# Kernel optimization log

Measured on AMD Instinct MI355X. Metric: run time of the kernel, lower is better.

The kernel has to match this reference:

```python
import jax, jax.numpy as jnp
import numpy as np

B, S, E, H = 4, 2048, 1024, 16
D = E // H  # head_dim


def setup_inputs() -> dict:
    key = jax.random.key(0)
    ks = jax.random.split(key, 7)
    scale = 1.0 / np.sqrt(E)
    return {
        "query": jax.random.normal(ks[0], (B, S, E), dtype=jnp.float32),
        "key": jax.random.normal(ks[1], (B, S, E), dtype=jnp.float32),
        "value": jax.random.normal(ks[2], (B, S, E), dtype=jnp.float32),
        "Wq": jax.random.normal(ks[3], (E, E), dtype=jnp.float32) * scale,
        "Wk": jax.random.normal(ks[4], (E, E), dtype=jnp.float32) * scale,
        "Wv": jax.random.normal(ks[5], (E, E), dtype=jnp.float32) * scale,
        "Wo": jax.random.normal(ks[6], (E, E), dtype=jnp.float32) * scale,
    }


def reference(query, key, value, Wq, Wk, Wv, Wo):
    b, s, e = query.shape
    sm_scale = (e // H) ** -0.5
    # TTLinear: x @ W.T; reshape to [b, h, s, d]
    q = (query @ Wq.T).reshape(b, s, H, D).transpose(0, 2, 1, 3)
    k = (key @ Wk.T).reshape(b, s, H, D).transpose(0, 2, 1, 3)
    v = (value @ Wv.T).reshape(b, s, H, D).transpose(0, 2, 1, 3)
    scores = jnp.einsum("bhqd,bhkd->bhqk", q, k) * sm_scale  # [b,h,s,s]
    attn = jax.nn.softmax(scores, axis=-1)
    out = jnp.einsum("bhqk,bhkd->bhqd", attn, v)
    out = out.transpose(0, 2, 1, 3).reshape(b, s, e)
    # dropout is identity in eval mode
    return out @ Wo.T
```

## Files before the change

kernel.cpp:

```cpp
#include <hip/hip_runtime.h>
#include <hip/hip_bf16.h>

#define BB 4
#define SS 2048
#define EE 1024
#define HH 16
#define DD 64
#define MM (BB*SS)

using f16x8 = __attribute__((ext_vector_type(8))) _Float16;
using f16x4 = __attribute__((ext_vector_type(4))) _Float16;
using f32x4 = __attribute__((ext_vector_type(4))) float;

typedef __attribute__((address_space(3))) void       as3_void;
typedef const __attribute__((address_space(1))) void as1_cvoid;

__device__ __forceinline__ void async16(void* lds, const void* g) {
    __builtin_amdgcn_global_load_lds((as1_cvoid*)g, (as3_void*)lds, 16, 0, 0);
}

__global__ __launch_bounds__(256) void cvt_kernel(const float* __restrict__ s,
                                                  _Float16* __restrict__ d, int n8) {
    int i = blockIdx.x * 256 + threadIdx.x;
    if (i < n8) {
        const float4* s4 = (const float4*)s;
        float4 v0 = s4[2 * i], v1 = s4[2 * i + 1];
        f16x8 h;
        h[0] = (_Float16)v0.x; h[1] = (_Float16)v0.y;
        h[2] = (_Float16)v0.z; h[3] = (_Float16)v0.w;
        h[4] = (_Float16)v1.x; h[5] = (_Float16)v1.y;
        h[6] = (_Float16)v1.z; h[7] = (_Float16)v1.w;
        ((f16x8*)d)[i] = h;
    }
}

template <typename TC>
__global__ __launch_bounds__(256) void gemm_bt_f16(const _Float16* __restrict__ A,
                                                   const _Float16* __restrict__ Bw,
                                                   TC* __restrict__ C,
                                                   int M, int N, int K) {
    constexpr int BM = 128, BN = 128, BK = 32;
    __shared__ alignas(16) _Float16 As[BM * BK];
    __shared__ alignas(16) _Float16 Bs[BN * BK];

    const int tid  = threadIdx.x;
    const int lane = tid & 63;
    const int wave = tid >> 6;
    const int wm   = (wave >> 1) * 64;
    const int wn   = (wave & 1) * 64;
    const int quad = lane >> 4;
    const int c    = lane & 15;
    const int m0   = blockIdx.x * BM;
    const int n0   = blockIdx.y * BN;

    f32x4 acc[4][4] = {};

    for (int k0 = 0; k0 < K; k0 += BK) {
#pragma unroll
        for (int p = 0; p < 2; ++p) {
            int idx = (p * 4 + wave) * 64 + lane;
            int row = idx >> 2, kc = (idx & 3) * 8;
            async16(As + (p * 4 + wave) * 512, A  + (size_t)(m0 + row) * K + k0 + kc);
            async16(Bs + (p * 4 + wave) * 512, Bw + (size_t)(n0 + row) * K + k0 + kc);
        }
        __syncthreads();

        f16x8 af[4], bf[4];
#pragma unroll
        for (int i = 0; i < 4; ++i)
            af[i] = *(const f16x8*)&As[(wm + i * 16 + c) * BK + quad * 8];
#pragma unroll
        for (int j = 0; j < 4; ++j)
            bf[j] = *(const f16x8*)&Bs[(wn + j * 16 + c) * BK + quad * 8];
#pragma unroll
        for (int i = 0; i < 4; ++i)
#pragma unroll
            for (int j = 0; j < 4; ++j)
                acc[i][j] = __builtin_amdgcn_mfma_f32_16x16x32_f16(af[i], bf[j], acc[i][j], 0, 0, 0);
        __syncthreads();
    }

#pragma unroll
    for (int i = 0; i < 4; ++i)
#pragma unroll
        for (int j = 0; j < 4; ++j)
#pragma unroll
            for (int r = 0; r < 4; ++r) {
                int row = m0 + wm + i * 16 + quad * 4 + r;
                int col = n0 + wn + j * 16 + c;
                C[(size_t)row * N + col] = (TC)acc[i][j][r];
            }
}

__global__ __launch_bounds__(256, 4) void attn_kernel(const _Float16* __restrict__ Q,
                                                      const _Float16* __restrict__ K,
                                                      const _Float16* __restrict__ V,
                                                      _Float16* __restrict__ O) {
    constexpr int KT = 64, LQ = 72, LK = 72, LV = 72, LP = 72;
    __shared__ alignas(16) _Float16 smem[(128 + 64 + 64) * 72];
    _Float16* Qs  = smem;
    _Float16* KPs = smem + 128 * 72;
    _Float16* Vts = smem + 192 * 72;

    const int tid  = threadIdx.x;
    const int lane = tid & 63;
    const int wave = tid >> 6;
    const int quad = lane >> 4;
    const int c    = lane & 15;
    const int bh   = blockIdx.y;
    const int b    = bh >> 4, h = bh & 15;
    const int q0   = blockIdx.x * 128;

    const _Float16* Qg = Q + (size_t)(b * SS + q0) * EE + h * DD;
    const _Float16* Kg = K + (size_t)(b * SS) * EE + h * DD;
    const _Float16* Vg = V + (size_t)(b * SS) * EE + h * DD;

#pragma unroll
    for (int p = 0; p < 4; ++p) {
        int ch = tid + p * 256;
        int row = ch >> 3, kc = (ch & 7) * 8;
        *(f16x8*)&Qs[row * LQ + kc] = *(const f16x8*)&Qg[(size_t)row * EE + kc];
    }

    const float cs = 0.125f * 1.44269504f;
    float m2[2] = {-INFINITY, -INFINITY};
    float l[2]  = {0.f, 0.f};
    f32x4 o_acc[2][4] = {};

    for (int s0 = 0; s0 < SS; s0 += KT) {
        __syncthreads();
#pragma unroll
        for (int p = 0; p < 2; ++p) {
            int ch = tid + p * 256;
            int row = ch >> 3, kc = (ch & 7) * 8;
            *(f16x8*)&KPs[row * LK + kc] = *(const f16x8*)&Kg[(size_t)(s0 + row) * EE + kc];
        }
#pragma unroll
        for (int p = 0; p < 2; ++p) {
            int ch = tid + p * 256;
            int d = ch & 63, scg = ch >> 6;
            f16x8 hv;
#pragma unroll
            for (int j = 0; j < 8; ++j)
                hv[j] = Vg[(size_t)(s0 + scg * 8 + j) * EE + d];
            *(f16x8*)&Vts[d * LV + scg * 8] = hv;
        }
        __syncthreads();

        f32x4 sacc[2][4] = {};
#pragma unroll
        for (int kt = 0; kt < 2; ++kt) {
            f16x8 ak[4], bq[2];
#pragma unroll
            for (int j = 0; j < 4; ++j)
                ak[j] = *(const f16x8*)&KPs[(j * 16 + c) * LK + kt * 32 + quad * 8];
#pragma unroll
            for (int i = 0; i < 2; ++i)
                bq[i] = *(const f16x8*)&Qs[(wave * 32 + i * 16 + c) * LQ + kt * 32 + quad * 8];
#pragma unroll
            for (int i = 0; i < 2; ++i)
#pragma unroll
                for (int j = 0; j < 4; ++j)
                    sacc[i][j] = __builtin_amdgcn_mfma_f32_16x16x32_f16(ak[j], bq[i], sacc[i][j], 0, 0, 0);
        }

#pragma unroll
        for (int i = 0; i < 2; ++i) {
            float mt = sacc[i][0][0];
#pragma unroll
            for (int j = 0; j < 4; ++j)
#pragma unroll
                for (int r = 0; r < 4; ++r) mt = fmaxf(mt, sacc[i][j][r]);
            mt = fmaxf(mt, __shfl_xor(mt, 16));
            mt = fmaxf(mt, __shfl_xor(mt, 32));
            float mnew = fmaxf(m2[i], mt * cs);
            float al   = __builtin_amdgcn_exp2f(m2[i] - mnew);
            m2[i] = mnew;
            float rs = 0.f;
#pragma unroll
            for (int j = 0; j < 4; ++j)
#pragma unroll
                for (int r = 0; r < 4; ++r) {
                    float pv = __builtin_amdgcn_exp2f(sacc[i][j][r] * cs - mnew);
                    sacc[i][j][r] = pv;
                    rs += pv;
                }
            rs += __shfl_xor(rs, 16);
            rs += __shfl_xor(rs, 32);
            l[i] = l[i] * al + rs;
#pragma unroll
            for (int dt = 0; dt < 4; ++dt)
#pragma unroll
                for (int r = 0; r < 4; ++r) o_acc[i][dt][r] *= al;
        }

        __syncthreads();

#pragma unroll
        for (int i = 0; i < 2; ++i) {
#pragma unroll
            for (int j = 0; j < 4; ++j) {
                f16x4 pw;
#pragma unroll
                for (int r = 0; r < 4; ++r) pw[r] = (_Float16)sacc[i][j][r];
                *(f16x4*)&KPs[(wave * 16 + c) * LP + j * 16 + quad * 4] = pw;
            }
#pragma unroll
            for (int kt = 0; kt < 2; ++kt) {
                f16x8 pb = *(const f16x8*)&KPs[(wave * 16 + c) * LP + kt * 32 + quad * 8];
#pragma unroll
                for (int dt = 0; dt < 4; ++dt) {
                    f16x8 av = *(const f16x8*)&Vts[(dt * 16 + c) * LV + kt * 32 + quad * 8];
                    o_acc[i][dt] = __builtin_amdgcn_mfma_f32_16x16x32_f16(av, pb, o_acc[i][dt], 0, 0, 0);
                }
            }
        }
    }

    _Float16* Og = O + (size_t)(b * SS + q0) * EE + h * DD;
#pragma unroll
    for (int i = 0; i < 2; ++i) {
        float inv = 1.0f / l[i];
#pragma unroll
        for (int dt = 0; dt < 4; ++dt) {
            f16x4 ov;
#pragma unroll
            for (int r = 0; r < 4; ++r) ov[r] = (_Float16)(o_acc[i][dt][r] * inv);
            *(f16x4*)&Og[(size_t)(wave * 32 + i * 16 + c) * EE + dt * 16 + quad * 4] = ov;
        }
    }
}

extern "C" void kernel_launch(void* const* d_in, const int* in_sizes, int n_in,
                              void* d_out, int out_size, void* d_ws, size_t ws_size,
                              hipStream_t stream) {
    const float* query = (const float*)d_in[0];
    const float* key   = (const float*)d_in[1];
    const float* value = (const float*)d_in[2];
    const float* Wq    = (const float*)d_in[3];
    const float* Wk    = (const float*)d_in[4];
    const float* Wv    = (const float*)d_in[5];
    const float* Wo    = (const float*)d_in[6];
    float* out = (float*)d_out;

    const size_t NE = (size_t)MM * EE;
    const size_t NW = (size_t)EE * EE;
    _Float16* buf0 = (_Float16*)d_ws;
    _Float16* Qw   = buf0 + NE;
    _Float16* Kw   = Qw + NE;
    _Float16* Vw   = Kw + NE;
    _Float16* wq   = Vw + NE;
    _Float16* wk   = wq + NW;
    _Float16* wv   = wk + NW;
    _Float16* wo   = wv + NW;

    dim3 gg(MM / 128, EE / 128);
    dim3 blk(256);
    const int actN8 = (int)(NE / 8), wN8 = (int)(NW / 8);

    cvt_kernel<<<wN8 / 256, blk, 0, stream>>>(Wq, wq, wN8);
    cvt_kernel<<<wN8 / 256, blk, 0, stream>>>(Wk, wk, wN8);
    cvt_kernel<<<wN8 / 256, blk, 0, stream>>>(Wv, wv, wN8);
    cvt_kernel<<<wN8 / 256, blk, 0, stream>>>(Wo, wo, wN8);

    cvt_kernel<<<actN8 / 256, blk, 0, stream>>>(query, buf0, actN8);
    gemm_bt_f16<_Float16><<<gg, blk, 0, stream>>>(buf0, wq, Qw, MM, EE, EE);
    cvt_kernel<<<actN8 / 256, blk, 0, stream>>>(key, buf0, actN8);
    gemm_bt_f16<_Float16><<<gg, blk, 0, stream>>>(buf0, wk, Kw, MM, EE, EE);
    cvt_kernel<<<actN8 / 256, blk, 0, stream>>>(value, buf0, actN8);
    gemm_bt_f16<_Float16><<<gg, blk, 0, stream>>>(buf0, wv, Vw, MM, EE, EE);

    attn_kernel<<<dim3(SS / 128, BB * HH), blk, 0, stream>>>(Qw, Kw, Vw, buf0);

    gemm_bt_f16<float><<<gg, blk, 0, stream>>>(buf0, wo, out, MM, EE, EE);
}
```

Baseline: 418.5 us.

## Fuse fp32-to-fp16 conversion into batched QKV GEMM and prefetch K/V in attention

The three Q/K/V projection GEMMs become one launch over a z-dimension. Each reads fp32 activations directly and converts them to fp16 while filling shared memory, so the separate activation conversion passes and their fp16 round trip through memory are gone. The four weight conversions are merged into a single launch. The attention kernel now prefetches the next K/V tile into registers during compute and loads the V fragments once, ahead of the softmax. The trade-off is that the A operand is no longer loaded asynchronously into shared memory, and each K step re-reads fp32 activations across the N tiles, which adds register pressure and load traffic inside the GEMM.

Result: slower. 502.4 us (+20.1%).

```diff
diff --git a/kernel.cpp b/kernel.cpp
--- a/kernel.cpp
+++ b/kernel.cpp
@@ -19,26 +19,34 @@
     __builtin_amdgcn_global_load_lds((as1_cvoid*)g, (as3_void*)lds, 16, 0, 0);
 }
 
-__global__ __launch_bounds__(256) void cvt_kernel(const float* __restrict__ s,
-                                                  _Float16* __restrict__ d, int n8) {
+__device__ __forceinline__ f16x8 cvt8(const float* src) {
+    const float4 v0 = *(const float4*)src;
+    const float4 v1 = *(const float4*)(src + 4);
+    f16x8 h;
+    h[0] = (_Float16)v0.x; h[1] = (_Float16)v0.y;
+    h[2] = (_Float16)v0.z; h[3] = (_Float16)v0.w;
+    h[4] = (_Float16)v1.x; h[5] = (_Float16)v1.y;
+    h[6] = (_Float16)v1.z; h[7] = (_Float16)v1.w;
+    return h;
+}
+
+__global__ __launch_bounds__(256) void cvt_w(const float* __restrict__ w0,
+                                             const float* __restrict__ w1,
+                                             const float* __restrict__ w2,
+                                             const float* __restrict__ w3,
+                                             _Float16* __restrict__ dst, int n8) {
+    const float* s = blockIdx.y == 0 ? w0 : blockIdx.y == 1 ? w1 : blockIdx.y == 2 ? w2 : w3;
+    _Float16* d = dst + (size_t)blockIdx.y * EE * EE;
     int i = blockIdx.x * 256 + threadIdx.x;
-    if (i < n8) {
-        const float4* s4 = (const float4*)s;
-        float4 v0 = s4[2 * i], v1 = s4[2 * i + 1];
-        f16x8 h;
-        h[0] = (_Float16)v0.x; h[1] = (_Float16)v0.y;
-        h[2] = (_Float16)v0.z; h[3] = (_Float16)v0.w;
-        h[4] = (_Float16)v1.x; h[5] = (_Float16)v1.y;
-        h[6] = (_Float16)v1.z; h[7] = (_Float16)v1.w;
-        ((f16x8*)d)[i] = h;
-    }
-}
-
-template <typename TC>
-__global__ __launch_bounds__(256) void gemm_bt_f16(const _Float16* __restrict__ A,
-                                                   const _Float16* __restrict__ Bw,
-                                                   TC* __restrict__ C,
-                                                   int M, int N, int K) {
+    if (i < n8) ((f16x8*)d)[i] = cvt8(s + i * 8);
+}
+
+__global__ __launch_bounds__(256) void gemm_qkv(const float* __restrict__ A0,
+                                                const float* __restrict__ A1,
+                                                const float* __restrict__ A2,
+                                                const _Float16* __restrict__ W,
+                                                _Float16* __restrict__ Cb,
+                                                int M, int N, int K) {
     constexpr int BM = 128, BN = 128, BK = 32;
     __shared__ alignas(16) _Float16 As[BM * BK];
     __shared__ alignas(16) _Float16 Bs[BN * BK];
@@ -52,6 +60,73 @@
     const int c    = lane & 15;
     const int m0   = blockIdx.x * BM;
     const int n0   = blockIdx.y * BN;
+    const int z    = blockIdx.z;
+
+    const float* A = z == 0 ? A0 : z == 1 ? A1 : A2;
+    const _Float16* Bw = W + (size_t)z * EE * EE;
+    _Float16* C = Cb + (size_t)z * MM * EE;
+
+    f32x4 acc[4][4] = {};
+
+    for (int k0 = 0; k0 < K; k0 += BK) {
+#pragma unroll
+        for (int p = 0; p < 2; ++p) {
+            int idx = (p * 4 + wave) * 64 + lane;
+            int row = idx >> 2, kc = (idx & 3) * 8;
+            async16(Bs + (p * 4 + wave) * 512, Bw + (size_t)(n0 + row) * K + k0 + kc);
+        }
+#pragma unroll
+        for (int p = 0; p < 2; ++p) {
+            int ch = tid + p * 256;
+            int row = ch >> 2, kc = (ch & 3) * 8;
+            *(f16x8*)&As[row * BK + kc] = cvt8(A + (size_t)(m0 + row) * K + k0 + kc);
+        }
+        __syncthreads();
+
+        f16x8 af[4], bf[4];
+#pragma unroll
+        for (int i = 0; i < 4; ++i)
+            af[i] = *(const f16x8*)&As[(wm + i * 16 + c) * BK + quad * 8];
+#pragma unroll
+        for (int j = 0; j < 4; ++j)
+            bf[j] = *(const f16x8*)&Bs[(wn + j * 16 + c) * BK + quad * 8];
+#pragma unroll
+        for (int i = 0; i < 4; ++i)
+#pragma unroll
+            for (int j = 0; j < 4; ++j)
+                acc[i][j] = __builtin_amdgcn_mfma_f32_16x16x32_f16(af[i], bf[j], acc[i][j], 0, 0, 0);
+        __syncthreads();
+    }
+
+#pragma unroll
+    for (int i = 0; i < 4; ++i)
+#pragma unroll
+        for (int j = 0; j < 4; ++j)
+#pragma unroll
+            for (int r = 0; r < 4; ++r) {
+                int row = m0 + wm + i * 16 + quad * 4 + r;
+                int col = n0 + wn + j * 16 + c;
+                C[(size_t)row * N + col] = (_Float16)acc[i][j][r];
+            }
+}
+
+__global__ __launch_bounds__(256) void gemm_bt_f16(const _Float16* __restrict__ A,
+                                                   const _Float16* __restrict__ Bw,
+                                                   float* __restrict__ C,
+                                                   int M, int N, int K) {
+    constexpr int BM = 128, BN = 128, BK = 32;
+    __shared__ alignas(16) _Float16 As[BM * BK];
+    __shared__ alignas(16) _Float16 Bs[BN * BK];
+
+    const int tid  = threadIdx.x;
+    const int lane = tid & 63;
+    const int wave = tid >> 6;
+    const int wm   = (wave >> 1) * 64;
+    const int wn   = (wave & 1) * 64;
+    const int quad = lane >> 4;
+    const int c    = lane & 15;
+    const int m0   = blockIdx.x * BM;
+    const int n0   = blockIdx.y * BN;
 
     f32x4 acc[4][4] = {};
 
@@ -88,7 +163,7 @@
             for (int r = 0; r < 4; ++r) {
                 int row = m0 + wm + i * 16 + quad * 4 + r;
                 int col = n0 + wn + j * 16 + c;
-                C[(size_t)row * N + col] = (TC)acc[i][j][r];
+                C[(size_t)row * N + col] = acc[i][j][r];
             }
 }
 
@@ -122,6 +197,23 @@
         *(f16x8*)&Qs[row * LQ + kc] = *(const f16x8*)&Qg[(size_t)row * EE + kc];
     }
 
+    f16x8 kreg[2], vreg[2];
+    auto load_kv = [&](int s0) {
+#pragma unroll
+        for (int p = 0; p < 2; ++p) {
+            int ch = tid + p * 256;
+            int row = ch >> 3, kc = (ch & 7) * 8;
+            kreg[p] = *(const f16x8*)&Kg[(size_t)(s0 + row) * EE + kc];
+            int d = ch & 63, scg = ch >> 6;
+            f16x8 hv;
+#pragma unroll
+            for (int j = 0; j < 8; ++j)
+                hv[j] = Vg[(size_t)(s0 + scg * 8 + j) * EE + d];
+            vreg[p] = hv;
+        }
+    };
+    load_kv(0);
+
     const float cs = 0.125f * 1.44269504f;
     float m2[2] = {-INFINITY, -INFINITY};
     float l[2]  = {0.f, 0.f};
@@ -133,19 +225,13 @@
         for (int p = 0; p < 2; ++p) {
             int ch = tid + p * 256;
             int row = ch >> 3, kc = (ch & 7) * 8;
-            *(f16x8*)&KPs[row * LK + kc] = *(const f16x8*)&Kg[(size_t)(s0 + row) * EE + kc];
-        }
-#pragma unroll
-        for (int p = 0; p < 2; ++p) {
-            int ch = tid + p * 256;
+            *(f16x8*)&KPs[row * LK + kc] = kreg[p];
             int d = ch & 63, scg = ch >> 6;
-            f16x8 hv;
-#pragma unroll
-            for (int j = 0; j < 8; ++j)
-                hv[j] = Vg[(size_t)(s0 + scg * 8 + j) * EE + d];
-            *(f16x8*)&Vts[d * LV + scg * 8] = hv;
-        }
-        __syncthreads();
+            *(f16x8*)&Vts[d * LV + scg * 8] = vreg[p];
+        }
+        __syncthreads();
+
+        if (s0 + KT < SS) load_kv(s0 + KT);
 
         f32x4 sacc[2][4] = {};
 #pragma unroll
@@ -163,6 +249,13 @@
                 for (int j = 0; j < 4; ++j)
                     sacc[i][j] = __builtin_amdgcn_mfma_f32_16x16x32_f16(ak[j], bq[i], sacc[i][j], 0, 0, 0);
         }
+
+        f16x8 av[2][4];
+#pragma unroll
+        for (int kt = 0; kt < 2; ++kt)
+#pragma unroll
+            for (int dt = 0; dt < 4; ++dt)
+                av[kt][dt] = *(const f16x8*)&Vts[(dt * 16 + c) * LV + kt * 32 + quad * 8];
 
 #pragma unroll
         for (int i = 0; i < 2; ++i) {
@@ -209,10 +302,8 @@
             for (int kt = 0; kt < 2; ++kt) {
                 f16x8 pb = *(const f16x8*)&KPs[(wave * 16 + c) * LP + kt * 32 + quad * 8];
 #pragma unroll
-                for (int dt = 0; dt < 4; ++dt) {
-                    f16x8 av = *(const f16x8*)&Vts[(dt * 16 + c) * LV + kt * 32 + quad * 8];
-                    o_acc[i][dt] = __builtin_amdgcn_mfma_f32_16x16x32_f16(av, pb, o_acc[i][dt], 0, 0, 0);
-                }
+                for (int dt = 0; dt < 4; ++dt)
+                    o_acc[i][dt] = __builtin_amdgcn_mfma_f32_16x16x32_f16(av[kt][dt], pb, o_acc[i][dt], 0, 0, 0);
             }
         }
     }
@@ -245,32 +336,19 @@
 
     const size_t NE = (size_t)MM * EE;
     const size_t NW = (size_t)EE * EE;
-    _Float16* buf0 = (_Float16*)d_ws;
-    _Float16* Qw   = buf0 + NE;
-    _Float16* Kw   = Qw + NE;
-    _Float16* Vw   = Kw + NE;
-    _Float16* wq   = Vw + NE;
-    _Float16* wk   = wq + NW;
-    _Float16* wv   = wk + NW;
-    _Float16* wo   = wv + NW;
-
-    dim3 gg(MM / 128, EE / 128);
+    _Float16* Qw = (_Float16*)d_ws;
+    _Float16* Kw = Qw + NE;
+    _Float16* Vw = Kw + NE;
+    _Float16* Wf = Vw + NE;
+
     dim3 blk(256);
-    const int actN8 = (int)(NE / 8), wN8 = (int)(NW / 8);
-
-    cvt_kernel<<<wN8 / 256, blk, 0, stream>>>(Wq, wq, wN8);
-    cvt_kernel<<<wN8 / 256, blk, 0, stream>>>(Wk, wk, wN8);
-    cvt_kernel<<<wN8 / 256, blk, 0, stream>>>(Wv, wv, wN8);
-    cvt_kernel<<<wN8 / 256, blk, 0, stream>>>(Wo, wo, wN8);
-
-    cvt_kernel<<<actN8 / 256, blk, 0, stream>>>(query, buf0, actN8);
-    gemm_bt_f16<_Float16><<<gg, blk, 0, stream>>>(buf0, wq, Qw, MM, EE, EE);
-    cvt_kernel<<<actN8 / 256, blk, 0, stream>>>(key, buf0, actN8);
-    gemm_bt_f16<_Float16><<<gg, blk, 0, stream>>>(buf0, wk, Kw, MM, EE, EE);
-    cvt_kernel<<<actN8 / 256, blk, 0, stream>>>(value, buf0, actN8);
-    gemm_bt_f16<_Float16><<<gg, blk, 0, stream>>>(buf0, wv, Vw, MM, EE, EE);
-
-    attn_kernel<<<dim3(SS / 128, BB * HH), blk, 0, stream>>>(Qw, Kw, Vw, buf0);
-
-    gemm_bt_f16<float><<<gg, blk, 0, stream>>>(buf0, wo, out, MM, EE, EE);
-}
+    const int wN8 = (int)(NW / 8);
+
+    cvt_w<<<dim3(wN8 / 256, 4), blk, 0, stream>>>(Wq, Wk, Wv, Wo, Wf, wN8);
+
+    gemm_qkv<<<dim3(MM / 128, EE / 128, 3), blk, 0, stream>>>(query, key, value, Wf, Qw, MM, EE, EE);
+
+    attn_kernel<<<dim3(SS / 128, BB * HH), blk, 0, stream>>>(Qw, Kw, Vw, Qw);
+
+    gemm_bt_f16<<<dim3(MM / 128, EE / 128), blk, 0, stream>>>(Qw, Wf + 3 * NW, out, MM, EE, EE);
+}
```
